# Performance work log

Hardware: AMD Instinct MI355X
Metric: run time of the kernel (lower is better)

The kernel has to match this reference:

```python
import jax, jax.numpy as jnp
import numpy as np

V, D, OUT, H, FF, L, K, POOL = 4097, 128, 64, 8, 256, 2, 9, 20
B, LE, LP = 32, 3000, 2000
GRID, WIDTH = 5, 257
DR = OUT // 8  # channel-attention reduction


def _ln(x, p):
    mu = jnp.mean(x, -1, keepdims=True)
    var = jnp.mean((x - mu) ** 2, -1, keepdims=True)
    return (x - mu) * jax.lax.rsqrt(var + 1e-5) * p[0] + p[1]


def _rope(x):
    # x: [B,H,S,hd], interleaved rotary embedding
    S, hd = x.shape[-2], x.shape[-1]
    inv = 1.0 / (10000.0 ** (jnp.arange(0, hd, 2, dtype=jnp.float32) / hd))
    ang = jnp.arange(S, dtype=jnp.float32)[:, None] * inv[None, :]  # [S,hd/2]
    c, s = jnp.cos(ang), jnp.sin(ang)
    x1, x2 = x[..., 0::2], x[..., 1::2]
    return jnp.stack([x1 * c - x2 * s, x1 * s + x2 * c], axis=-1).reshape(x.shape)


def _cbat_layer(x, qkv_w, qkv_b, o_w, o_b, ca_w1, ca_w2, sa_w,
                ff1_w, ff1_b, ff2_w, ff2_b, ln1, ln2):
    # x: [B,S,d] (batch-first inside CBAT, matching x.permute(1,0,2) in torch)
    Bx, S, d = x.shape
    hd = d // H

    def proj(i):
        return (x @ qkv_w[i] + qkv_b[i]).reshape(Bx, S, H, hd).transpose(0, 2, 1, 3)

    q, k, v = proj(0), proj(1), proj(2)
    q, k = _rope(q), _rope(k)
    attn = jax.nn.softmax(jnp.einsum('bhqd,bhkd->bhqk', q, k) / jnp.sqrt(jnp.float32(hd)), axis=-1)
    ctx = jnp.einsum('bhqk,bhkd->bhqd', attn, v).transpose(0, 2, 1, 3).reshape(Bx, S, d)
    # CBAM-style channel attention (pool over sequence)
    avg, mx = ctx.mean(1), ctx.max(1)  # [B,d]
    ca = jax.nn.sigmoid(jax.nn.relu(avg @ ca_w1) @ ca_w2 + jax.nn.relu(mx @ ca_w1) @ ca_w2)
    ctx = ctx * ca[:, None, :]
    # CBAM-style spatial attention (pool over channels, conv over sequence)
    feat = jnp.stack([ctx.mean(-1), ctx.max(-1)], axis=1)  # [B,2,S]
    sa = jax.nn.sigmoid(jax.lax.conv_general_dilated(
        feat, sa_w[None], (1,), 'SAME', dimension_numbers=('NCH', 'OIH', 'NCH')))  # [B,1,S]
    ctx = ctx * sa.transpose(0, 2, 1)
    out = ctx @ o_w + o_b
    aloss = jnp.mean(attn ** 2)  # adaptive attention regularizer
    x = _ln(x + out, ln1)
    ff = jax.nn.relu(x @ ff1_w + ff1_b) @ ff2_w + ff2_b
    x = _ln(x + ff, ln2)
    return x, aloss


def _mha(q_in, k_in, v_in, in_w, in_b, out_w, out_b):
    # torch nn.MultiheadAttention math (batch-first layout here; math identical)
    d = q_in.shape[-1]
    hd = d // H
    Wq, Wk, Wv = jnp.split(in_w, 3, 0)
    bq, bk, bv = jnp.split(in_b, 3, 0)

    def heads(t):
        return t.reshape(t.shape[0], t.shape[1], H, hd).transpose(0, 2, 1, 3)

    q, k, v = heads(q_in @ Wq.T + bq), heads(k_in @ Wk.T + bk), heads(v_in @ Wv.T + bv)
    attn = jax.nn.softmax(jnp.einsum('bhqd,bhkd->bhqk', q, k) / jnp.sqrt(jnp.float32(hd)), axis=-1)
    ctx = jnp.einsum('bhqk,bhkd->bhqd', attn, v).transpose(0, 2, 1, 3).reshape(q_in.shape)
    return ctx @ out_w.T + out_b


def _fourier(x, wc, ws, b):
    # FourierKAN layer: sum_k a*cos(kx) + b*sin(kx)
    kx = x[:, :, None] * jnp.arange(1, GRID + 1, dtype=x.dtype)  # [B,in,g]
    return jnp.einsum('big,oig->bo', jnp.cos(kx), wc) + jnp.einsum('big,oig->bo', jnp.sin(kx), ws) + b


def _frontend(ids, emb, conv_w, conv_b, bn):
    x = emb[ids]  # [B,Lseq,D]
    x = jax.lax.conv_general_dilated(x.transpose(0, 2, 1), conv_w, (1,), 'VALID',
                                     dimension_numbers=('NCH', 'OIH', 'NCH')) + conv_b[None, :, None]
    x = jax.nn.relu(x)
    x = jax.lax.reduce_window(x, -jnp.inf, jax.lax.max, (1, 1, POOL), (1, 1, POOL), 'VALID')
    g, be, mu, var = bn[0], bn[1], bn[2], bn[3]  # BatchNorm1d (eval mode)
    x = (x - mu[None, :, None]) * jax.lax.rsqrt(var[None, :, None] + 1e-5) * g[None, :, None] + be[None, :, None]
    return x.transpose(0, 2, 1)  # [B,S,OUT]


def _forward(enhancer_ids, promoter_ids, emb_en, emb_pr, conv_w_en, conv_b_en, conv_w_pr, conv_b_pr,
             bn_en, bn_pr, t_qkv_w, t_qkv_b, t_o_w, t_o_b, t_ca_w1, t_ca_w2, t_sa_w,
             t_ff1_w, t_ff1_b, t_ff2_w, t_ff2_b, t_ln1, t_ln2,
             cross_in_w, cross_in_b, cross_out_w, cross_out_b,
             self_in_w, self_in_b, self_out_w, self_out_b,
             fk1_c, fk1_s, fk1_b, fk2_c, fk2_s, fk2_b):
    en = _frontend(enhancer_ids, emb_en, conv_w_en, conv_b_en, bn_en)
    pr = _frontend(promoter_ids, emb_pr, conv_w_pr, conv_b_pr, bn_pr)
    total_aloss = jnp.float32(0.0)
    branches = [en, pr]
    for s in range(2):  # 0=enhancer stack, 1=promoter stack
        x = branches[s]
        for l in range(L):
            x, al = _cbat_layer(x, t_qkv_w[s, l], t_qkv_b[s, l], t_o_w[s, l], t_o_b[s, l],
                                t_ca_w1[s, l], t_ca_w2[s, l], t_sa_w[s, l],
                                t_ff1_w[s, l], t_ff1_b[s, l], t_ff2_w[s, l], t_ff2_b[s, l],
                                t_ln1[s, l], t_ln2[s, l])
            total_aloss = total_aloss + al
        branches[s] = x
    en, pr = branches
    en_att = _mha(en, pr, pr, cross_in_w, cross_in_b, cross_out_w, cross_out_b)
    en_fin = _mha(en_att, en_att, en_att, self_in_w, self_in_b, self_out_w, self_out_b)
    pr_fin = _mha(pr, pr, pr, self_in_w, self_in_b, self_out_w, self_out_b)
    combined = jnp.concatenate([en_fin.mean(1), pr_fin.mean(1)], axis=1)  # AdaptiveAvgPool1d(1)
    hidden = _fourier(combined, fk1_c, fk1_s, fk1_b)
    result = _fourier(hidden, fk2_c, fk2_s, fk2_b)
    return jax.nn.sigmoid(result), combined, total_aloss


def setup_inputs() -> dict:
    key = jax.random.key(0)
    ks = iter(jax.random.split(key, 64))

    def nrm(shape, sc=0.02):
        return jax.random.normal(next(ks), shape, jnp.float32) * sc

    ln_init = lambda: jnp.stack([jnp.ones((2, L, OUT)), jnp.zeros((2, L, OUT))], axis=2)
    inp = {
        'enhancer_ids': jax.random.randint(next(ks), (B, LE), 0, V),
        'promoter_ids': jax.random.randint(next(ks), (B, LP), 0, V),
        'enhancer_features': jax.random.normal(next(ks), (B, 10), jnp.float32),
        'promoter_features': jax.random.normal(next(ks), (B, 10), jnp.float32),
        'emb_en': nrm((V, D), 0.1), 'emb_pr': nrm((V, D), 0.1),
        'conv_w_en': nrm((OUT, D, K)), 'conv_b_en': jnp.zeros((OUT,)),
        'conv_w_pr': nrm((OUT, D, K)), 'conv_b_pr': jnp.zeros((OUT,)),
        'bn_en': jnp.stack([jnp.ones(OUT), jnp.zeros(OUT), jnp.zeros(OUT), jnp.ones(OUT)]),
        'bn_pr': jnp.stack([jnp.ones(OUT), jnp.zeros(OUT), jnp.zeros(OUT), jnp.ones(OUT)]),
        't_qkv_w': nrm((2, L, 3, OUT, OUT)), 't_qkv_b': jnp.zeros((2, L, 3, OUT)),
        't_o_w': nrm((2, L, OUT, OUT)), 't_o_b': jnp.zeros((2, L, OUT)),
        't_ca_w1': nrm((2, L, OUT, DR)), 't_ca_w2': nrm((2, L, DR, OUT)),
        't_sa_w': nrm((2, L, 2, 7)),
        't_ff1_w': nrm((2, L, OUT, FF)), 't_ff1_b': jnp.zeros((2, L, FF)),
        't_ff2_w': nrm((2, L, FF, OUT)), 't_ff2_b': jnp.zeros((2, L, OUT)),
        't_ln1': ln_init(), 't_ln2': ln_init(),
        'cross_in_w': nrm((3 * OUT, OUT)), 'cross_in_b': jnp.zeros((3 * OUT,)),
        'cross_out_w': nrm((OUT, OUT)), 'cross_out_b': jnp.zeros((OUT,)),
        'self_in_w': nrm((3 * OUT, OUT)), 'self_in_b': jnp.zeros((3 * OUT,)),
        'self_out_w': nrm((OUT, OUT)), 'self_out_b': jnp.zeros((OUT,)),
        'fk1_c': nrm((WIDTH, 2 * OUT, GRID), 0.1), 'fk1_s': nrm((WIDTH, 2 * OUT, GRID), 0.1),
        'fk1_b': jnp.zeros((WIDTH,)),
        'fk2_c': nrm((1, WIDTH, GRID), 0.1), 'fk2_s': nrm((1, WIDTH, GRID), 0.1),
        'fk2_b': jnp.zeros((1,)),
    }
    return inp


def reference(enhancer_ids, promoter_ids, enhancer_features, promoter_features,
              emb_en, emb_pr, conv_w_en, conv_b_en, conv_w_pr, conv_b_pr,
              bn_en, bn_pr, t_qkv_w, t_qkv_b, t_o_w, t_o_b, t_ca_w1, t_ca_w2, t_sa_w,
              t_ff1_w, t_ff1_b, t_ff2_w, t_ff2_b, t_ln1, t_ln2,
              cross_in_w, cross_in_b, cross_out_w, cross_out_b,
              self_in_w, self_in_b, self_out_w, self_out_b,
              fk1_c, fk1_s, fk1_b, fk2_c, fk2_s, fk2_b):
    # enhancer_features / promoter_features are accepted but unused by the original forward
    return _forward(enhancer_ids, promoter_ids, emb_en, emb_pr, conv_w_en, conv_b_en,
                    conv_w_pr, conv_b_pr, bn_en, bn_pr, t_qkv_w, t_qkv_b, t_o_w, t_o_b,
                    t_ca_w1, t_ca_w2, t_sa_w, t_ff1_w, t_ff1_b, t_ff2_w, t_ff2_b, t_ln1, t_ln2,
                    cross_in_w, cross_in_b, cross_out_w, cross_out_b,
                    self_in_w, self_in_b, self_out_w, self_out_b,
                    fk1_c, fk1_s, fk1_b, fk2_c, fk2_s, fk2_b)
```

## Files before the change

### kernel.cpp

```cpp
#include <hip/hip_runtime.h>
#include <math.h>

#define BB 32
#define SE 149
#define SP 99
#define LE_LEN 3000
#define LP_LEN 2000
#define VT 8
#define ROWS_EN (BB * SE)
#define ROWS_PR (BB * SP)
#define ROWS_ALL (ROWS_EN + ROWS_PR)

__device__ __forceinline__ void row_decode(int row, int& branch, int& b,
                                           int& s, int& S, int& lrow) {
  if (row < ROWS_EN) { branch = 0; S = SE; lrow = row; b = row / SE; s = row - b * SE; }
  else { branch = 1; S = SP; lrow = row - ROWS_EN; b = lrow / SP; s = lrow - b * SP; }
}

__global__ __launch_bounds__(256) void prep_kernel(
    const float* __restrict__ cw_en, const float* __restrict__ cw_pr,
    const float* __restrict__ cross_in, const float* __restrict__ cross_out,
    const float* __restrict__ self_in, const float* __restrict__ self_out,
    float* __restrict__ W2en, float* __restrict__ W2pr,
    float* __restrict__ Wt, float* __restrict__ Al) {
  int bb = blockIdx.x;
  if (bb == 0 && threadIdx.x == 0) Al[0] = 0.f;
  if (bb < 576) {
    const float* src = (bb < 288) ? cw_en : cw_pr;
    float* dst = (bb < 288) ? W2en : W2pr;
    int i = ((bb < 288) ? bb : bb - 288) * 256 + threadIdx.x;
    int oc = i / 1152, r = i % 1152, ic = r / 9, k = r % 9;
    dst[ic * 576 + k * 64 + oc] = src[i];
  } else {
    int m = bb - 576;
    const float* src = (m < 3) ? cross_in + m * 4096
                     : (m == 3) ? cross_out
                     : (m < 7) ? self_in + (m - 4) * 4096
                     : self_out;
    for (int i = threadIdx.x; i < 4096; i += 256) {
      int o = i >> 6, c = i & 63;
      Wt[m * 4096 + c * 64 + o] = src[i];
    }
  }
}
// ... 3 lines not shown
    const float* __restrict__ W2en, const float* __restrict__ W2pr,
    float* __restrict__ Cen, float* __restrict__ Cpr) {
  int blk = blockIdx.x;
  int branch = (blk >= 513);
  const float* emb = branch ? emb_pr : emb_en;
  const float* W2 = branch ? W2pr : W2en;
  float* C = branch ? Cpr : Cen;
  int v0 = (branch ? blk - 513 : blk) * VT;
  __shared__ float e[VT][128];
  int t = threadIdx.x;
  int nv = 4097 - v0; if (nv > VT) nv = VT;
  for (int i = t; i < nv * 128; i += 192) e[i >> 7][i & 127] = emb[v0 * 128 + i];
  __syncthreads();
  float a0[VT], a1[VT], a2[VT];
#pragma unroll
  for (int v = 0; v < VT; ++v) { a0[v] = 0.f; a1[v] = 0.f; a2[v] = 0.f; }
  for (int ic = 0; ic < 128; ++ic) {
    float w0 = W2[ic * 576 + t];
    float w1 = W2[ic * 576 + t + 192];
    float w2 = W2[ic * 576 + t + 384];
#pragma unroll
    for (int v = 0; v < VT; ++v) {
      float ev = e[v][ic];
      a0[v] += ev * w0; a1[v] += ev * w1; a2[v] += ev * w2;
    }
  }
  for (int v = 0; v < nv; ++v) {
    C[(size_t)(v0 + v) * 576 + t] = a0[v];
    C[(size_t)(v0 + v) * 576 + t + 192] = a1[v];
    C[(size_t)(v0 + v) * 576 + t + 384] = a2[v];
  }
}

__global__ __launch_bounds__(256) void frontend_kernel(
    const int* __restrict__ en_ids, const int* __restrict__ pr_ids,
    const float* __restrict__ Cen, const float* __restrict__ Cpr,
    const float* __restrict__ cb_en, const float* __restrict__ cb_pr,
    const float* __restrict__ bn_en, const float* __restrict__ bn_pr,
    float* __restrict__ Xen, float* __restrict__ Xpr) {
  int t = threadIdx.x;
  int wid = t >> 6, oc = t & 63;
  int row = blockIdx.x * 4 + wid;
  int branch, b, s, S, lrow;
  row_decode(row, branch, b, s, S, lrow);
  const int* ids = branch ? pr_ids : en_ids;
  int Lin = branch ? LP_LEN : LE_LEN;
  const float* C = branch ? Cpr : Cen;
  const float* cb = branch ? cb_pr : cb_en;
  const float* bn = branch ? bn_pr : bn_en;
  float* X = branch ? Xpr : Xen;
  __shared__ int idl[4][28];
  if (oc < 28) idl[wid][oc] = ids[b * Lin + s * 20 + oc];
  __syncthreads();
  float bias = cb[oc];
  float m = -INFINITY;
  for (int p = 0; p < 20; ++p) {
    float acc = bias;
#pragma unroll
    for (int k = 0; k < 9; ++k) acc += C[idl[wid][p + k] * 576 + k * 64 + oc];
    acc = fmaxf(acc, 0.f);
    m = fmaxf(m, acc);
  }
  float g = bn[oc], be = bn[64 + oc], mu = bn[128 + oc], var = bn[192 + oc];
  X[(size_t)lrow * 64 + oc] = (m - mu) * rsqrtf(var + 1e-5f) * g + be;
}

__global__ __launch_bounds__(256) void qkv_rope_kernel(
    const float* __restrict__ Xen, const float* __restrict__ Xpr,
    const float* __restrict__ t_qkv_w, const float* __restrict__ t_qkv_b, int l,
    float* __restrict__ Q, float* __restrict__ K, float* __restrict__ V) {
  int t = threadIdx.x;
  int wid = t >> 6, oc = t & 63;
  int row = blockIdx.x * 4 + wid;
  int branch, b, s, S, lrow;
  row_decode(row, branch, b, s, S, lrow);
  const float* X = branch ? Xpr : Xen;
  int idx = branch * 2 + l;
  const float* W = t_qkv_w + (size_t)idx * 3 * 4096;
  const float* bias = t_qkv_b + idx * 192;
  __shared__ float xr[4][64], qs[4][64], ks[4][64];
  xr[wid][oc] = X[lrow * 64 + oc];
  __syncthreads();
  float q = bias[oc], k = bias[64 + oc], v = bias[128 + oc];
  for (int c = 0; c < 64; ++c) {
    float xc = xr[wid][c];
    q += xc * W[c * 64 + oc];
    k += xc * W[4096 + c * 64 + oc];
    v += xc * W[8192 + c * 64 + oc];
  }
  qs[wid][oc] = q; ks[wid][oc] = k;
  V[row * 64 + oc] = v;
  __syncthreads();
  int j = oc & 7;
  int p = j >> 1;
  float inv = powf(10000.f, -(float)p * 0.25f);
  float ang = (float)s * inv;
  float cc = cosf(ang), ss = sinf(ang);
  float qo, ko;
  if ((j & 1) == 0) {
    qo = qs[wid][oc] * cc - qs[wid][oc + 1] * ss;
    ko = ks[wid][oc] * cc - ks[wid][oc + 1] * ss;
  } else {
    qo = qs[wid][oc - 1] * ss + qs[wid][oc] * cc;
    ko = ks[wid][oc - 1] * ss + ks[wid][oc] * cc;
  }
  Q[row * 64 + oc] = qo;
  K[row * 64 + oc] = ko;
}

__global__ __launch_bounds__(256) void attn_kernel(
    const float* __restrict__ Q, const float* __restrict__ K,
    const float* __restrict__ V, float* __restrict__ ctx,
    int nblk0, int Sq0, int Sk0, int qb0, int kb0, float als0,
    int Sq1, int Sk1, int qb1, int kb1, float als1,
    float* __restrict__ aloss_acc) {
  int blk = blockIdx.x;
// ... 24 lines not shown
      for (int j = 0; j < 8; ++j) sdot += q[j] * kk[kki * 8 + j];
      sdot *= sc;
      if (sdot > m) {
        float f = expf(m - sdot);
        sum *= f; sum2 *= f * f;
#pragma unroll
        for (int j = 0; j < 8; ++j) acc[j] *= f;
        m = sdot;
      }
      float e = expf(sdot - m);
      sum += e; sum2 += e * e;
#pragma unroll
      for (int j = 0; j < 8; ++j) acc[j] += e * vv[kki * 8 + j];
    }
    float invs = 1.f / sum;
#pragma unroll
    for (int j = 0; j < 8; ++j)
      ctx[(qb + b * Sq + t) * 64 + h * 8 + j] = acc[j] * invs;
    rowsum2 = sum2 * invs * invs;
  }
  if (als != 0.f) {
    float wsum = rowsum2;
    for (int off = 32; off; off >>= 1) wsum += __shfl_down(wsum, off, 64);
    __shared__ float wred[4];
    if ((t & 63) == 0) wred[t >> 6] = wsum;
    __syncthreads();
    if (t == 0) {
      float tot = wred[0] + wred[1] + wred[2] + wred[3];
      atomicAdd(aloss_acc, tot * als);
    }
  }
}

__global__ __launch_bounds__(512) void ca_kernel(
    const float* __restrict__ ctx, const float* __restrict__ t_ca_w1,
    const float* __restrict__ t_ca_w2, int l, float* __restrict__ ca) {
  int bp = blockIdx.x;
  int branch = bp >> 5, b = bp & 31;
  int S = branch ? SP : SE;
  int base = branch ? ROWS_EN : 0;
  int idx = branch * 2 + l;
  const float* W1 = t_ca_w1 + idx * 512;
  const float* W2 = t_ca_w2 + idx * 512;
  int t = threadIdx.x;
  int c = t & 63, seg = t >> 6;
  float sum = 0.f, mx = -INFINITY;
  for (int s = seg; s < S; s += 8) {
    float v = ctx[(base + b * S + s) * 64 + c];
    sum += v; mx = fmaxf(mx, v);
  }
  __shared__ float ssum[8][64], smx[8][64];
  ssum[seg][c] = sum; smx[seg][c] = mx;
  __syncthreads();
  __shared__ float avg_l[64], mx_l[64], ha[8], hm[8];
  if (t < 64) {
    float a = 0.f, m = -INFINITY;
#pragma unroll
    for (int g = 0; g < 8; ++g) { a += ssum[g][t]; m = fmaxf(m, smx[g][t]); }
    avg_l[t] = a / (float)S; mx_l[t] = m;
  }
  __syncthreads();
  if (t < 8) {
    float a = 0.f, m2 = 0.f;
    for (int i = 0; i < 64; ++i) {
      a += avg_l[i] * W1[i * 8 + t];
      m2 += mx_l[i] * W1[i * 8 + t];
    }
    ha[t] = fmaxf(a, 0.f); hm[t] = fmaxf(m2, 0.f);
  }
  __syncthreads();
  if (t < 64) {
    float o = 0.f;
#pragma unroll
    for (int j = 0; j < 8; ++j) o += (ha[j] + hm[j]) * W2[j * 64 + t];
    ca[bp * 64 + t] = 1.f / (1.f + expf(-o));
  }
}

__global__ __launch_bounds__(256) void feat_kernel(
    float* __restrict__ ctx, const float* __restrict__ ca,
    float* __restrict__ fmean, float* __restrict__ fmax) {
  int row = blockIdx.x * 4 + (threadIdx.x >> 6);
  int branch, b, s, S, lrow;
  row_decode(row, branch, b, s, S, lrow);
  int c = threadIdx.x & 63;
  float v = ctx[row * 64 + c] * ca[(branch * 32 + b) * 64 + c];
  ctx[row * 64 + c] = v;
  float sum = v, mx = v;
  for (int off = 32; off; off >>= 1) {
    sum += __shfl_xor(sum, off, 64);
    mx = fmaxf(mx, __shfl_xor(mx, off, 64));
  }
  if (c == 0) { fmean[row] = sum * (1.f / 64.f); fmax[row] = mx; }
}

__global__ __launch_bounds__(256) void tail_kernel(
    const float* __restrict__ ctx, const float* __restrict__ fmean,
    const float* __restrict__ fmax, const float* __restrict__ t_sa_w,
    const float* __restrict__ t_o_w, const float* __restrict__ t_o_b,
    const float* __restrict__ t_ln1, const float* __restrict__ t_ff1_w,
    const float* __restrict__ t_ff1_b, const float* __restrict__ t_ff2_w,
    const float* __restrict__ t_ff2_b, const float* __restrict__ t_ln2,
    int l, float* __restrict__ Xen, float* __restrict__ Xpr) {
  int t = threadIdx.x;
  int wid = t >> 6, lane = t & 63;
  int row = blockIdx.x * 4 + wid;
  int branch, b, s, S, lrow;
  row_decode(row, branch, b, s, S, lrow);
  int idx = branch * 2 + l;
  const float* sa_w = t_sa_w + idx * 14;
  float sa = 0.f;
  if (lane == 0) {
    for (int k = 0; k < 7; ++k) {
      int p = s + k - 3;
      if (p >= 0 && p < S)
        sa += fmean[row - s + p] * sa_w[k] + fmax[row - s + p] * sa_w[7 + k];
    }
    sa = 1.f / (1.f + expf(-sa));
  }
  sa = __shfl(sa, 0, 64);
  __shared__ float rowv[4][64], xr[4][64], h[4][256];
  rowv[wid][lane] = ctx[row * 64 + lane] * sa;
  __syncthreads();
  const float* o_w = t_o_w + (size_t)idx * 4096;
  float o = t_o_b[idx * 64 + lane];
  for (int c = 0; c < 64; ++c) o += rowv[wid][c] * o_w[c * 64 + lane];
  float* X = branch ? Xpr : Xen;
  float r = X[lrow * 64 + lane] + o;
  float mu = r;
  for (int of = 32; of; of >>= 1) mu += __shfl_xor(mu, of, 64);
  mu *= (1.f / 64.f);
  float d = r - mu;
  float var = d * d;
  for (int of = 32; of; of >>= 1) var += __shfl_xor(var, of, 64);
  var *= (1.f / 64.f);
  const float* ln1 = t_ln1 + idx * 128;
  float x1 = d * rsqrtf(var + 1e-5f) * ln1[lane] + ln1[64 + lane];
  xr[wid][lane] = x1;
  __syncthreads();
  const float* W1 = t_ff1_w + (size_t)idx * 16384;
  float a0 = t_ff1_b[idx * 256 + t], a1 = a0, a2 = a0, a3 = a0;
  for (int c = 0; c < 64; ++c) {
    float w = W1[c * 256 + t];
    a0 += xr[0][c] * w; a1 += xr[1][c] * w; a2 += xr[2][c] * w; a3 += xr[3][c] * w;
  }
  h[0][t] = fmaxf(a0, 0.f); h[1][t] = fmaxf(a1, 0.f);
  h[2][t] = fmaxf(a2, 0.f); h[3][t] = fmaxf(a3, 0.f);
  __syncthreads();
  const float* W2 = t_ff2_w + (size_t)idx * 16384;
  float o2 = t_ff2_b[idx * 64 + lane];
  for (int j = 0; j < 256; ++j) o2 += h[wid][j] * W2[j * 64 + lane];
  float r2 = x1 + o2;
  mu = r2;
  for (int of = 32; of; of >>= 1) mu += __shfl_xor(mu, of, 64);
  mu *= (1.f / 64.f);
  d = r2 - mu;
  var = d * d;
  for (int of = 32; of; of >>= 1) var += __shfl_xor(var, of, 64);
  var *= (1.f / 64.f);
  const float* ln2 = t_ln2 + idx * 128;
  X[lrow * 64 + lane] = d * rsqrtf(var + 1e-5f) * ln2[lane] + ln2[64 + lane];
}

__global__ __launch_bounds__(256) void cross_proj_kernel(
    const float* __restrict__ Xen, const float* __restrict__ Xpr,
    const float* __restrict__ Wt, const float* __restrict__ bias,
    float* __restrict__ Q, float* __restrict__ K, float* __restrict__ V) {
  int t = threadIdx.x;
  int wid = t >> 6, oc = t & 63;
  int blk = blockIdx.x;
  __shared__ float xr[4][64];
  if (blk < ROWS_EN / 4) {
    int row = blk * 4 + wid;
    xr[wid][oc] = Xen[row * 64 + oc];
    __syncthreads();
    float o = bias[oc];
    for (int c = 0; c < 64; ++c) o += xr[wid][c] * Wt[c * 64 + oc];
    Q[row * 64 + oc] = o;
  } else {
    int lr = (blk - ROWS_EN / 4) * 4 + wid;
    xr[wid][oc] = Xpr[lr * 64 + oc];
    __syncthreads();
    float k = bias[64 + oc], v = bias[128 + oc];
    for (int c = 0; c < 64; ++c) {
      float xc = xr[wid][c];
      k += xc * Wt[4096 + c * 64 + oc];
      v += xc * Wt[8192 + c * 64 + oc];
    }
    K[(ROWS_EN + lr) * 64 + oc] = k;
    V[(ROWS_EN + lr) * 64 + oc] = v;
  }
}

__global__ __launch_bounds__(256) void self_qkv_kernel(
    const float* __restrict__ inEn, const float* __restrict__ inPr,
    const float* __restrict__ Wt, const float* __restrict__ bias,
    float* __restrict__ Q, float* __restrict__ K, float* __restrict__ V) {
  int t = threadIdx.x;
  int wid = t >> 6, oc = t & 63;
  int row = blockIdx.x * 4 + wid;
  const float* in; int lrow;
  if (row < ROWS_EN) { in = inEn; lrow = row; }
  else { in = inPr; lrow = row - ROWS_EN; }
  __shared__ float xr[4][64];
  xr[wid][oc] = in[lrow * 64 + oc];
  __syncthreads();
  float q = bias[oc], k = bias[64 + oc], v = bias[128 + oc];
  for (int c = 0; c < 64; ++c) {
    float xc = xr[wid][c];
    q += xc * Wt[c * 64 + oc];
    k += xc * Wt[4096 + c * 64 + oc];
    v += xc * Wt[8192 + c * 64 + oc];
  }
  Q[row * 64 + oc] = q;
  K[row * 64 + oc] = k;
  V[row * 64 + oc] = v;
}

__global__ __launch_bounds__(256) void dual_proj_kernel(
    const float* __restrict__ in, const float* __restrict__ Wt,
    const float* __restrict__ bias, float* __restrict__ out0,
    float* __restrict__ out1) {
  int t = threadIdx.x;
  int wid = t >> 6, oc = t & 63;
  int row = blockIdx.x * 4 + wid;
  float* out; int lrow;
  if (row < ROWS_EN) { out = out0; lrow = row; }
  else { out = out1; lrow = row - ROWS_EN; }
  __shared__ float xr[4][64];
  xr[wid][oc] = in[row * 64 + oc];
  __syncthreads();
  float o = bias[oc];
  for (int c = 0; c < 64; ++c) o += xr[wid][c] * Wt[c * 64 + oc];
  out[lrow * 64 + oc] = o;
}

__global__ __launch_bounds__(512) void mean_trig_kernel(
    const float* __restrict__ en_fin, const float* __restrict__ pr_fin,
    float* __restrict__ comb, float* __restrict__ trig) {
  int b = blockIdx.x;
  int t = threadIdx.x;
  int col = t & 127, seg = t >> 7;
  float sum = 0.f;
  if (col < 64) {
    for (int s = seg; s < SE; s += 4) sum += en_fin[(b * SE + s) * 64 + col];
  } else {
    int c = col - 64;
    for (int s = seg; s < SP; s += 4) sum += pr_fin[(b * SP + s) * 64 + c];
  }
  __shared__ float red[4][128];
  __shared__ float comb_s[128];
  red[seg][col] = sum;
  __syncthreads();
  if (t < 128) {
    float tot = red[0][t] + red[1][t] + red[2][t] + red[3][t];
    float cv = tot / (t < 64 ? (float)SE : (float)SP);
    comb_s[t] = cv;
    comb[b * 128 + t] = cv;
  }
  __syncthreads();
  for (int i = t; i < 640; i += 512) {
    int ii = i / 5, g = i - ii * 5;
    float x = comb_s[ii] * (float)(g + 1);
    trig[b * 1280 + i] = cosf(x);
    trig[b * 1280 + 640 + i] = sinf(x);
  }
}

__global__ __launch_bounds__(256) void fourier1_kernel(
    const float* __restrict__ trig, const float* __restrict__ wc,
    const float* __restrict__ ws, const float* __restrict__ bias,
    float* __restrict__ hidden) {
  int b = blockIdx.x;
  int t = threadIdx.x;
  int wid = t >> 6, lane = t & 63;
  int o = blockIdx.y * 4 + wid;
  if (o >= 257) return;
  const float* ct = trig + b * 1280;
  const float* st = ct + 640;
  float acc = 0.f;
  for (int i = lane; i < 640; i += 64)
    acc += ct[i] * wc[o * 640 + i] + st[i] * ws[o * 640 + i];
  for (int off = 32; off; off >>= 1) acc += __shfl_xor(acc, off, 64);
  if (lane == 0) hidden[b * 257 + o] = acc + bias[o];
}

__global__ void fourier2_kernel(const float* __restrict__ hidden,
                                const float* __restrict__ wc,
                                const float* __restrict__ ws,
                                const float* __restrict__ bias,
                                const float* __restrict__ aloss_acc,
                                float* __restrict__ out) {
  int b = blockIdx.x;
  int t = threadIdx.x;
  float acc = 0.f;
  if (t < 257) {
    float x = hidden[b * 257 + t];
#pragma unroll
    for (int g = 0; g < 5; ++g) {
      float a = x * (float)(g + 1);
      acc += cosf(a) * wc[t * 5 + g] + sinf(a) * ws[t * 5 + g];
    }
  }
  for (int off = 32; off; off >>= 1) acc += __shfl_xor(acc, off, 64);
  __shared__ float wred[5];
  if ((t & 63) == 0) wred[t >> 6] = acc;
  __syncthreads();
  if (t == 0) {
    float tot = wred[0] + wred[1] + wred[2] + wred[3] + wred[4] + bias[0];
    out[b] = 1.f / (1.f + expf(-tot));
    if (b == 0) out[4128] = aloss_acc[0];
  }
}

extern "C" void kernel_launch(void* const* d_in, const int* in_sizes, int n_in,
                              void* d_out, int out_size, void* d_ws, size_t ws_size,
                              hipStream_t stream) {
  const int* en_ids = (const int*)d_in[0];
  const int* pr_ids = (const int*)d_in[1];
  const float* emb_en = (const float*)d_in[4];
  const float* emb_pr = (const float*)d_in[5];
  const float* conv_w_en = (const float*)d_in[6];
  const float* conv_b_en = (const float*)d_in[7];
  const float* conv_w_pr = (const float*)d_in[8];
  const float* conv_b_pr = (const float*)d_in[9];
  const float* bn_en = (const float*)d_in[10];
  const float* bn_pr = (const float*)d_in[11];
  const float* t_qkv_w = (const float*)d_in[12];
  const float* t_qkv_b = (const float*)d_in[13];
  const float* t_o_w = (const float*)d_in[14];
  const float* t_o_b = (const float*)d_in[15];
  const float* t_ca_w1 = (const float*)d_in[16];
  const float* t_ca_w2 = (const float*)d_in[17];
  const float* t_sa_w = (const float*)d_in[18];
  const float* t_ff1_w = (const float*)d_in[19];
  const float* t_ff1_b = (const float*)d_in[20];
  const float* t_ff2_w = (const float*)d_in[21];
  const float* t_ff2_b = (const float*)d_in[22];
  const float* t_ln1 = (const float*)d_in[23];
  const float* t_ln2 = (const float*)d_in[24];
  const float* cross_in_w = (const float*)d_in[25];
  const float* cross_in_b = (const float*)d_in[26];
  const float* cross_out_w = (const float*)d_in[27];
  const float* cross_out_b = (const float*)d_in[28];
  const float* self_in_w = (const float*)d_in[29];
  const float* self_in_b = (const float*)d_in[30];
  const float* self_out_w = (const float*)d_in[31];
  const float* self_out_b = (const float*)d_in[32];
  const float* fk1_c = (const float*)d_in[33];
  const float* fk1_s = (const float*)d_in[34];
  const float* fk1_b = (const float*)d_in[35];
  const float* fk2_c = (const float*)d_in[36];
  const float* fk2_s = (const float*)d_in[37];
  const float* fk2_b = (const float*)d_in[38];

  float* out = (float*)d_out;
  float* ws = (float*)d_ws;
  size_t off = 0;
  float* Cen = ws + off;  off += (size_t)4097 * 576;
  float* Cpr = ws + off;  off += (size_t)4097 * 576;
  float* W2en = ws + off; off += 73728;
  float* W2pr = ws + off; off += 73728;
  float* Wt = ws + off;   off += 8 * 4096;
  float* Xen = ws + off;  off += (size_t)ROWS_EN * 64;
  float* Xpr = ws + off;  off += (size_t)ROWS_PR * 64;
  float* Qb = ws + off;   off += (size_t)ROWS_ALL * 64;
  float* Kb = ws + off;   off += (size_t)ROWS_ALL * 64;
  float* Vb = ws + off;   off += (size_t)ROWS_ALL * 64;
  float* Ctx = ws + off;  off += (size_t)ROWS_ALL * 64;
  float* AttEn = ws + off; off += (size_t)ROWS_EN * 64;
  float* PrFin = ws + off; off += (size_t)ROWS_PR * 64;
  float* Fm = ws + off;   off += ROWS_ALL;
  float* Fx = ws + off;   off += ROWS_ALL;
  float* CaB = ws + off;  off += 2 * BB * 64;
  float* Hid = ws + off;  off += BB * 257;
  float* Trig = ws + off; off += (size_t)BB * 1280;
  float* Al = ws + off;   off += 8;

  const float als_en = 1.f / ((float)BB * 8.f * (float)SE * (float)SE);
  const float als_pr = 1.f / ((float)BB * 8.f * (float)SP * (float)SP);

  prep_kernel<<<584, 256, 0, stream>>>(conv_w_en, conv_w_pr, cross_in_w,
                                       cross_out_w, self_in_w, self_out_w,
                                       W2en, W2pr, Wt, Al);
  conv_table_kernel<<<1026, 192, 0, stream>>>(emb_en, emb_pr, W2en, W2pr, Cen, Cpr);
  frontend_kernel<<<ROWS_ALL / 4, 256, 0, stream>>>(en_ids, pr_ids, Cen, Cpr,
                                                    conv_b_en, conv_b_pr, bn_en,
                                                    bn_pr, Xen, Xpr);

  for (int l = 0; l < 2; ++l) {
    qkv_rope_kernel<<<ROWS_ALL / 4, 256, 0, stream>>>(Xen, Xpr, t_qkv_w,
                                                      t_qkv_b, l, Qb, Kb, Vb);
    attn_kernel<<<512, 256, 0, stream>>>(Qb, Kb, Vb, Ctx,
                                         256, SE, SE, 0, 0, als_en,
                                         SP, SP, ROWS_EN, ROWS_EN, als_pr, Al);
    ca_kernel<<<64, 512, 0, stream>>>(Ctx, t_ca_w1, t_ca_w2, l, CaB);
    feat_kernel<<<ROWS_ALL / 4, 256, 0, stream>>>(Ctx, CaB, Fm, Fx);
    tail_kernel<<<ROWS_ALL / 4, 256, 0, stream>>>(
        Ctx, Fm, Fx, t_sa_w, t_o_w, t_o_b, t_ln1, t_ff1_w, t_ff1_b,
        t_ff2_w, t_ff2_b, t_ln2, l, Xen, Xpr);
  }

  cross_proj_kernel<<<ROWS_ALL / 4, 256, 0, stream>>>(Xen, Xpr, Wt,
                                                      cross_in_b, Qb, Kb, Vb);
  attn_kernel<<<256, 256, 0, stream>>>(Qb, Kb, Vb, Ctx,
                                       256, SE, SP, 0, ROWS_EN, 0.f,
                                       0, 0, 0, 0, 0.f, Al);
  dual_proj_kernel<<<ROWS_EN / 4, 256, 0, stream>>>(Ctx, Wt + 3 * 4096,
                                                    cross_out_b, AttEn, AttEn);

  self_qkv_kernel<<<ROWS_ALL / 4, 256, 0, stream>>>(AttEn, Xpr, Wt + 4 * 4096,
                                                    self_in_b, Qb, Kb, Vb);
  attn_kernel<<<512, 256, 0, stream>>>(Qb, Kb, Vb, Ctx,
                                       256, SE, SE, 0, 0, 0.f,
                                       SP, SP, ROWS_EN, ROWS_EN, 0.f, Al);
  dual_proj_kernel<<<ROWS_ALL / 4, 256, 0, stream>>>(Ctx, Wt + 7 * 4096,
                                                     self_out_b, Xen, PrFin);

  mean_trig_kernel<<<BB, 512, 0, stream>>>(Xen, PrFin, out + 32, Trig);
  fourier1_kernel<<<dim3(BB, 65), 256, 0, stream>>>(Trig, fk1_c, fk1_s,
                                                    fk1_b, Hid);
  fourier2_kernel<<<BB, 320, 0, stream>>>(Hid, fk2_c, fk2_s, fk2_b, Al, out);
}
```

Baseline: 362.4 us.

## Fuse per-row projection kernels into neighbours and merge head kernels

Folds the QKV+RoPE projection into the frontend and tail kernels, and merges channel attention with the feature pass. It also computes promoter self-attention QKV early so the promoter self-attention runs in the same launch as the cross attention. The three classifier-head kernels are collapsed into one. The aim is fewer launches and fewer global round trips of intermediate activations. In exchange it adds larger workspace buffers, more register and shared-memory use per kernel, and per-batch serial work in the fused head and cafeat kernels.

Result: slower. 531.2 us (+46.6%).

```diff
diff --git a/kernel.cpp b/kernel.cpp
--- a/kernel.cpp
+++ b/kernel.cpp
@@ -10,6 +10,7 @@
 #define ROWS_EN (BB * SE)
 #define ROWS_PR (BB * SP)
 #define ROWS_ALL (ROWS_EN + ROWS_PR)
+#define ROWS_EXT (ROWS_ALL + ROWS_PR)
 
 __device__ __forceinline__ void row_decode(int row, int& branch, int& b,
                                            int& s, int& S, int& lrow) {
@@ -79,12 +80,14 @@
   }
 }
 
-__global__ __launch_bounds__(256) void frontend_kernel(
+__global__ __launch_bounds__(256) void frontqkv_kernel(
     const int* __restrict__ en_ids, const int* __restrict__ pr_ids,
     const float* __restrict__ Cen, const float* __restrict__ Cpr,
     const float* __restrict__ cb_en, const float* __restrict__ cb_pr,
     const float* __restrict__ bn_en, const float* __restrict__ bn_pr,
-    float* __restrict__ Xen, float* __restrict__ Xpr) {
+    const float* __restrict__ t_qkv_w, const float* __restrict__ t_qkv_b,
+    float* __restrict__ Xen, float* __restrict__ Xpr,
+    float* __restrict__ Q, float* __restrict__ K, float* __restrict__ V) {
   int t = threadIdx.x;
   int wid = t >> 6, oc = t & 63;
   int row = blockIdx.x * 4 + wid;
@@ -97,6 +100,7 @@
   const float* bn = branch ? bn_pr : bn_en;
   float* X = branch ? Xpr : Xen;
   __shared__ int idl[4][28];
+  __shared__ float xr[4][64], qs[4][64], ks[4][64];
   if (oc < 28) idl[wid][oc] = ids[b * Lin + s * 20 + oc];
   __syncthreads();
   float bias = cb[oc];
@@ -109,26 +113,14 @@
     m = fmaxf(m, acc);
   }
   float g = bn[oc], be = bn[64 + oc], mu = bn[128 + oc], var = bn[192 + oc];
-  X[(size_t)lrow * 64 + oc] = (m - mu) * rsqrtf(var + 1e-5f) * g + be;
-}
-
-__global__ __launch_bounds__(256) void qkv_rope_kernel(
-    const float* __restrict__ Xen, const float* __restrict__ Xpr,
-    const float* __restrict__ t_qkv_w, const float* __restrict__ t_qkv_b, int l,
-    float* __restrict__ Q, float* __restrict__ K, float* __restrict__ V) {
-  int t = threadIdx.x;
-  int wid = t >> 6, oc = t & 63;
-  int row = blockIdx.x * 4 + wid;
-  int branch, b, s, S, lrow;
-  row_decode(row, branch, b, s, S, lrow);
-  const float* X = branch ? Xpr : Xen;
-  int idx = branch * 2 + l;
+  float xv = (m - mu) * rsqrtf(var + 1e-5f) * g + be;
+  X[(size_t)lrow * 64 + oc] = xv;
+  xr[wid][oc] = xv;
+  __syncthreads();
+  int idx = branch * 2;
   const float* W = t_qkv_w + (size_t)idx * 3 * 4096;
-  const float* bias = t_qkv_b + idx * 192;
-  __shared__ float xr[4][64], qs[4][64], ks[4][64];
-  xr[wid][oc] = X[lrow * 64 + oc];
-  __syncthreads();
-  float q = bias[oc], k = bias[64 + oc], v = bias[128 + oc];
+  const float* qb_ = t_qkv_b + idx * 192;
+  float q = qb_[oc], k = qb_[64 + oc], v = qb_[128 + oc];
   for (int c = 0; c < 64; ++c) {
     float xc = xr[wid][c];
     q += xc * W[c * 64 + oc];
@@ -219,9 +211,10 @@
   }
 }
 
-__global__ __launch_bounds__(512) void ca_kernel(
-    const float* __restrict__ ctx, const float* __restrict__ t_ca_w1,
-    const float* __restrict__ t_ca_w2, int l, float* __restrict__ ca) {
+__global__ __launch_bounds__(512) void cafeat_kernel(
+    float* __restrict__ ctx, const float* __restrict__ t_ca_w1,
+    const float* __restrict__ t_ca_w2, int l,
+    float* __restrict__ fmean, float* __restrict__ fmax) {
   int bp = blockIdx.x;
   int branch = bp >> 5, b = bp & 31;
   int S = branch ? SP : SE;
@@ -233,13 +226,13 @@
   int c = t & 63, seg = t >> 6;
   float sum = 0.f, mx = -INFINITY;
   for (int s = seg; s < S; s += 8) {
-    float v = ctx[(base + b * S + s) * 64 + c];
+    float v = ctx[(size_t)(base + b * S + s) * 64 + c];
     sum += v; mx = fmaxf(mx, v);
   }
   __shared__ float ssum[8][64], smx[8][64];
   ssum[seg][c] = sum; smx[seg][c] = mx;
   __syncthreads();
-  __shared__ float avg_l[64], mx_l[64], ha[8], hm[8];
+  __shared__ float avg_l[64], mx_l[64], ha[8], hm[8], ca_s[64];
   if (t < 64) {
     float a = 0.f, m = -INFINITY;
 #pragma unroll
@@ -260,35 +253,33 @@
     float o = 0.f;
 #pragma unroll
     for (int j = 0; j < 8; ++j) o += (ha[j] + hm[j]) * W2[j * 64 + t];
-    ca[bp * 64 + t] = 1.f / (1.f + expf(-o));
-  }
-}
-
-__global__ __launch_bounds__(256) void feat_kernel(
-    float* __restrict__ ctx, const float* __restrict__ ca,
-    float* __restrict__ fmean, float* __restrict__ fmax) {
-  int row = blockIdx.x * 4 + (threadIdx.x >> 6);
-  int branch, b, s, S, lrow;
-  row_decode(row, branch, b, s, S, lrow);
-  int c = threadIdx.x & 63;
-  float v = ctx[row * 64 + c] * ca[(branch * 32 + b) * 64 + c];
-  ctx[row * 64 + c] = v;
-  float sum = v, mx = v;
-  for (int off = 32; off; off >>= 1) {
-    sum += __shfl_xor(sum, off, 64);
-    mx = fmaxf(mx, __shfl_xor(mx, off, 64));
-  }
-  if (c == 0) { fmean[row] = sum * (1.f / 64.f); fmax[row] = mx; }
-}
-
-__global__ __launch_bounds__(256) void tail_kernel(
+    ca_s[t] = 1.f / (1.f + expf(-o));
+  }
+  __syncthreads();
+  float cav = ca_s[c];
+  for (int s = seg; s < S; s += 8) {
+    int grow = base + b * S + s;
+    float v = ctx[(size_t)grow * 64 + c] * cav;
+    ctx[(size_t)grow * 64 + c] = v;
+    float su = v, mv = v;
+    for (int off = 32; off; off >>= 1) {
+      su += __shfl_xor(su, off, 64);
+      mv = fmaxf(mv, __shfl_xor(mv, off, 64));
+    }
+    if (c == 0) { fmean[grow] = su * (1.f / 64.f); fmax[grow] = mv; }
+  }
+}
+
+__global__ __launch_bounds__(256) void tailqkv_kernel(
     const float* __restrict__ ctx, const float* __restrict__ fmean,
     const float* __restrict__ fmax, const float* __restrict__ t_sa_w,
     const float* __restrict__ t_o_w, const float* __restrict__ t_o_b,
     const float* __restrict__ t_ln1, const float* __restrict__ t_ff1_w,
     const float* __restrict__ t_ff1_b, const float* __restrict__ t_ff2_w,
     const float* __restrict__ t_ff2_b, const float* __restrict__ t_ln2,
-    int l, float* __restrict__ Xen, float* __restrict__ Xpr) {
+    int l, float* __restrict__ Xen, float* __restrict__ Xpr,
+    const float* __restrict__ t_qkv_w, const float* __restrict__ t_qkv_b,
+    float* __restrict__ Q, float* __restrict__ K, float* __restrict__ V) {
   int t = threadIdx.x;
   int wid = t >> 6, lane = t & 63;
   int row = blockIdx.x * 4 + wid;
@@ -306,14 +297,14 @@
     sa = 1.f / (1.f + expf(-sa));
   }
   sa = __shfl(sa, 0, 64);
-  __shared__ float rowv[4][64], xr[4][64], h[4][256];
-  rowv[wid][lane] = ctx[row * 64 + lane] * sa;
+  __shared__ float rowv[4][64], xr[4][64], h[4][256], qs[4][64], ks[4][64];
+  rowv[wid][lane] = ctx[(size_t)row * 64 + lane] * sa;
   __syncthreads();
   const float* o_w = t_o_w + (size_t)idx * 4096;
   float o = t_o_b[idx * 64 + lane];
   for (int c = 0; c < 64; ++c) o += rowv[wid][c] * o_w[c * 64 + lane];
   float* X = branch ? Xpr : Xen;
-  float r = X[lrow * 64 + lane] + o;
+  float r = X[(size_t)lrow * 64 + lane] + o;
   float mu = r;
   for (int of = 32; of; of >>= 1) mu += __shfl_xor(mu, of, 64);
   mu *= (1.f / 64.f);
@@ -346,155 +337,241 @@
   for (int of = 32; of; of >>= 1) var += __shfl_xor(var, of, 64);
   var *= (1.f / 64.f);
   const float* ln2 = t_ln2 + idx * 128;
-  X[lrow * 64 + lane] = d * rsqrtf(var + 1e-5f) * ln2[lane] + ln2[64 + lane];
-}
-
-__global__ __launch_bounds__(256) void cross_proj_kernel(
-    const float* __restrict__ Xen, const float* __restrict__ Xpr,
-    const float* __restrict__ Wt, const float* __restrict__ bias,
+  float fv = d * rsqrtf(var + 1e-5f) * ln2[lane] + ln2[64 + lane];
+  X[(size_t)lrow * 64 + lane] = fv;
+  xr[wid][lane] = fv;
+  __syncthreads();
+  int idx2 = branch * 2 + l + 1;
+  const float* W = t_qkv_w + (size_t)idx2 * 3 * 4096;
+  const float* qb_ = t_qkv_b + idx2 * 192;
+  float q = qb_[lane], k = qb_[64 + lane], v = qb_[128 + lane];
+  for (int c = 0; c < 64; ++c) {
+    float xc = xr[wid][c];
+    q += xc * W[c * 64 + lane];
+    k += xc * W[4096 + c * 64 + lane];
+    v += xc * W[8192 + c * 64 + lane];
+  }
+  qs[wid][lane] = q; ks[wid][lane] = k;
+  V[(size_t)row * 64 + lane] = v;
+  __syncthreads();
+  int j = lane & 7;
+  int p = j >> 1;
+  float inv = powf(10000.f, -(float)p * 0.25f);
+  float ang = (float)s * inv;
+  float cc = cosf(ang), ss = sinf(ang);
+  float qo, ko;
+  if ((j & 1) == 0) {
+    qo = qs[wid][lane] * cc - qs[wid][lane + 1] * ss;
+    ko = ks[wid][lane] * cc - ks[wid][lane + 1] * ss;
+  } else {
+    qo = qs[wid][lane - 1] * ss + qs[wid][lane] * cc;
+    ko = ks[wid][lane - 1] * ss + ks[wid][lane] * cc;
+  }
+  Q[(size_t)row * 64 + lane] = qo;
+  K[(size_t)row * 64 + lane] = ko;
+}
+
+__global__ __launch_bounds__(256) void tailcross_kernel(
+    const float* __restrict__ ctx, const float* __restrict__ fmean,
+    const float* __restrict__ fmax, const float* __restrict__ t_sa_w,
+    const float* __restrict__ t_o_w, const float* __restrict__ t_o_b,
+    const float* __restrict__ t_ln1, const float* __restrict__ t_ff1_w,
+    const float* __restrict__ t_ff1_b, const float* __restrict__ t_ff2_w,
+    const float* __restrict__ t_ff2_b, const float* __restrict__ t_ln2,
+    float* __restrict__ Xen, float* __restrict__ Xpr,
+    const float* __restrict__ Wt, const float* __restrict__ cib,
+    const float* __restrict__ sib,
     float* __restrict__ Q, float* __restrict__ K, float* __restrict__ V) {
   int t = threadIdx.x;
-  int wid = t >> 6, oc = t & 63;
-  int blk = blockIdx.x;
-  __shared__ float xr[4][64];
-  if (blk < ROWS_EN / 4) {
-    int row = blk * 4 + wid;
-    xr[wid][oc] = Xen[row * 64 + oc];
-    __syncthreads();
-    float o = bias[oc];
-    for (int c = 0; c < 64; ++c) o += xr[wid][c] * Wt[c * 64 + oc];
-    Q[row * 64 + oc] = o;
+  int wid = t >> 6, lane = t & 63;
+  int row = blockIdx.x * 4 + wid;
+  int branch, b, s, S, lrow;
+  row_decode(row, branch, b, s, S, lrow);
+  int idx = branch * 2 + 1;
+  const float* sa_w = t_sa_w + idx * 14;
+  float sa = 0.f;
+  if (lane == 0) {
+    for (int k = 0; k < 7; ++k) {
+      int p = s + k - 3;
+      if (p >= 0 && p < S)
+        sa += fmean[row - s + p] * sa_w[k] + fmax[row - s + p] * sa_w[7 + k];
+    }
+    sa = 1.f / (1.f + expf(-sa));
+  }
+  sa = __shfl(sa, 0, 64);
+  __shared__ float rowv[4][64], xr[4][64], h[4][256];
+  rowv[wid][lane] = ctx[(size_t)row * 64 + lane] * sa;
+  __syncthreads();
+  const float* o_w = t_o_w + (size_t)idx * 4096;
+  float o = t_o_b[idx * 64 + lane];
+  for (int c = 0; c < 64; ++c) o += rowv[wid][c] * o_w[c * 64 + lane];
+  float* X = branch ? Xpr : Xen;
+  float r = X[(size_t)lrow * 64 + lane] + o;
+  float mu = r;
+  for (int of = 32; of; of >>= 1) mu += __shfl_xor(mu, of, 64);
+  mu *= (1.f / 64.f);
+  float d = r - mu;
+  float var = d * d;
+  for (int of = 32; of; of >>= 1) var += __shfl_xor(var, of, 64);
+  var *= (1.f / 64.f);
+  const float* ln1 = t_ln1 + idx * 128;
+  float x1 = d * rsqrtf(var + 1e-5f) * ln1[lane] + ln1[64 + lane];
+  xr[wid][lane] = x1;
+  __syncthreads();
+  const float* W1 = t_ff1_w + (size_t)idx * 16384;
+  float a0 = t_ff1_b[idx * 256 + t], a1 = a0, a2 = a0, a3 = a0;
+  for (int c = 0; c < 64; ++c) {
+    float w = W1[c * 256 + t];
+    a0 += xr[0][c] * w; a1 += xr[1][c] * w; a2 += xr[2][c] * w; a3 += xr[3][c] * w;
+  }
+  h[0][t] = fmaxf(a0, 0.f); h[1][t] = fmaxf(a1, 0.f);
+  h[2][t] = fmaxf(a2, 0.f); h[3][t] = fmaxf(a3, 0.f);
+  __syncthreads();
+  const float* W2 = t_ff2_w + (size_t)idx * 16384;
+  float o2 = t_ff2_b[idx * 64 + lane];
+  for (int j = 0; j < 256; ++j) o2 += h[wid][j] * W2[j * 64 + lane];
+  float r2 = x1 + o2;
+  mu = r2;
+  for (int of = 32; of; of >>= 1) mu += __shfl_xor(mu, of, 64);
+  mu *= (1.f / 64.f);
+  d = r2 - mu;
+  var = d * d;
+  for (int of = 32; of; of >>= 1) var += __shfl_xor(var, of, 64);
+  var *= (1.f / 64.f);
+  const float* ln2 = t_ln2 + idx * 128;
+  float fv = d * rsqrtf(var + 1e-5f) * ln2[lane] + ln2[64 + lane];
+  X[(size_t)lrow * 64 + lane] = fv;
+  xr[wid][lane] = fv;
+  __syncthreads();
+  if (branch == 0) {
+    float q = cib[lane];
+    for (int c = 0; c < 64; ++c) q += xr[wid][c] * Wt[c * 64 + lane];
+    Q[(size_t)row * 64 + lane] = q;
   } else {
-    int lr = (blk - ROWS_EN / 4) * 4 + wid;
-    xr[wid][oc] = Xpr[lr * 64 + oc];
-    __syncthreads();
-    float k = bias[64 + oc], v = bias[128 + oc];
+    float k = cib[64 + lane], v = cib[128 + lane];
+    float q2 = sib[lane], k2 = sib[64 + lane], v2 = sib[128 + lane];
     for (int c = 0; c < 64; ++c) {
       float xc = xr[wid][c];
-      k += xc * Wt[4096 + c * 64 + oc];
-      v += xc * Wt[8192 + c * 64 + oc];
-    }
-    K[(ROWS_EN + lr) * 64 + oc] = k;
-    V[(ROWS_EN + lr) * 64 + oc] = v;
-  }
-}
-
-__global__ __launch_bounds__(256) void self_qkv_kernel(
-    const float* __restrict__ inEn, const float* __restrict__ inPr,
-    const float* __restrict__ Wt, const float* __restrict__ bias,
+      k += xc * Wt[4096 + c * 64 + lane];
+      v += xc * Wt[8192 + c * 64 + lane];
+      q2 += xc * Wt[4 * 4096 + c * 64 + lane];
+      k2 += xc * Wt[5 * 4096 + c * 64 + lane];
+      v2 += xc * Wt[6 * 4096 + c * 64 + lane];
+    }
+    K[(size_t)(ROWS_EN + lrow) * 64 + lane] = k;
+    V[(size_t)(ROWS_EN + lrow) * 64 + lane] = v;
+    Q[(size_t)(ROWS_ALL + lrow) * 64 + lane] = q2;
+    K[(size_t)(ROWS_ALL + lrow) * 64 + lane] = k2;
+    V[(size_t)(ROWS_ALL + lrow) * 64 + lane] = v2;
+  }
+}
+
+__global__ __launch_bounds__(256) void crossout_selfqkv_kernel(
+    const float* __restrict__ ctx, const float* __restrict__ Wt,
+    const float* __restrict__ cob, const float* __restrict__ sib,
     float* __restrict__ Q, float* __restrict__ K, float* __restrict__ V) {
   int t = threadIdx.x;
-  int wid = t >> 6, oc = t & 63;
+  int wid = t >> 6, lane = t & 63;
   int row = blockIdx.x * 4 + wid;
-  const float* in; int lrow;
-  if (row < ROWS_EN) { in = inEn; lrow = row; }
-  else { in = inPr; lrow = row - ROWS_EN; }
+  __shared__ float xr[4][64], att[4][64];
+  xr[wid][lane] = ctx[(size_t)row * 64 + lane];
+  __syncthreads();
+  float o = cob[lane];
+  for (int c = 0; c < 64; ++c) o += xr[wid][c] * Wt[3 * 4096 + c * 64 + lane];
+  att[wid][lane] = o;
+  __syncthreads();
+  float q = sib[lane], k = sib[64 + lane], v = sib[128 + lane];
+  for (int c = 0; c < 64; ++c) {
+    float xc = att[wid][c];
+    q += xc * Wt[4 * 4096 + c * 64 + lane];
+    k += xc * Wt[5 * 4096 + c * 64 + lane];
+    v += xc * Wt[6 * 4096 + c * 64 + lane];
+  }
+  Q[(size_t)row * 64 + lane] = q;
+  K[(size_t)row * 64 + lane] = k;
+  V[(size_t)row * 64 + lane] = v;
+}
+
+__global__ __launch_bounds__(256) void final_out_kernel(
+    const float* __restrict__ ctx, const float* __restrict__ Wt,
+    const float* __restrict__ sob, float* __restrict__ Xen,
+    float* __restrict__ PrFin) {
+  int t = threadIdx.x;
+  int wid = t >> 6, lane = t & 63;
+  int row = blockIdx.x * 4 + wid;
+  const float* src;
+  float* dst;
+  int lrow;
+  if (row < ROWS_EN) { src = ctx + (size_t)row * 64; dst = Xen; lrow = row; }
+  else { lrow = row - ROWS_EN; src = ctx + (size_t)(ROWS_ALL + lrow) * 64; dst = PrFin; }
   __shared__ float xr[4][64];
-  xr[wid][oc] = in[lrow * 64 + oc];
-  __syncthreads();
-  float q = bias[oc], k = bias[64 + oc], v = bias[128 + oc];
-  for (int c = 0; c < 64; ++c) {
-    float xc = xr[wid][c];
-    q += xc * Wt[c * 64 + oc];
-    k += xc * Wt[4096 + c * 64 + oc];
-    v += xc * Wt[8192 + c * 64 + oc];
-  }
-  Q[row * 64 + oc] = q;
-  K[row * 64 + oc] = k;
-  V[row * 64 + oc] = v;
-}
-
-__global__ __launch_bounds__(256) void dual_proj_kernel(
-    const float* __restrict__ in, const float* __restrict__ Wt,
-    const float* __restrict__ bias, float* __restrict__ out0,
-    float* __restrict__ out1) {
-  int t = threadIdx.x;
-  int wid = t >> 6, oc = t & 63;
-  int row = blockIdx.x * 4 + wid;
-  float* out; int lrow;
-  if (row < ROWS_EN) { out = out0; lrow = row; }
-  else { out = out1; lrow = row - ROWS_EN; }
-  __shared__ float xr[4][64];
-  xr[wid][oc] = in[row * 64 + oc];
-  __syncthreads();
-  float o = bias[oc];
-  for (int c = 0; c < 64; ++c) o += xr[wid][c] * Wt[c * 64 + oc];
-  out[lrow * 64 + oc] = o;
-}
-
-__global__ __launch_bounds__(512) void mean_trig_kernel(
+  xr[wid][lane] = src[lane];
+  __syncthreads();
+  float o = sob[lane];
+  for (int c = 0; c < 64; ++c) o += xr[wid][c] * Wt[7 * 4096 + c * 64 + lane];
+  dst[(size_t)lrow * 64 + lane] = o;
+}
+
+__global__ __launch_bounds__(512) void headfuse_kernel(
     const float* __restrict__ en_fin, const float* __restrict__ pr_fin,
-    float* __restrict__ comb, float* __restrict__ trig) {
+    const float* __restrict__ wc1, const float* __restrict__ ws1,
+    const float* __restrict__ b1, const float* __restrict__ wc2,
+    const float* __restrict__ ws2, const float* __restrict__ b2,
+    const float* __restrict__ aloss_acc, float* __restrict__ out) {
   int b = blockIdx.x;
   int t = threadIdx.x;
-  int col = t & 127, seg = t >> 7;
-  float sum = 0.f;
-  if (col < 64) {
-    for (int s = seg; s < SE; s += 4) sum += en_fin[(b * SE + s) * 64 + col];
-  } else {
-    int c = col - 64;
-    for (int s = seg; s < SP; s += 4) sum += pr_fin[(b * SP + s) * 64 + c];
-  }
-  __shared__ float red[4][128];
-  __shared__ float comb_s[128];
-  red[seg][col] = sum;
+  __shared__ float red[4][128], comb_s[128], ct[640], st[640], hid[257], wred[8];
+  {
+    int col = t & 127, seg = t >> 7;
+    float sum = 0.f;
+    if (col < 64) {
+      for (int s = seg; s < SE; s += 4) sum += en_fin[(size_t)(b * SE + s) * 64 + col];
+    } else {
+      int c = col - 64;
+      for (int s = seg; s < SP; s += 4) sum += pr_fin[(size_t)(b * SP + s) * 64 + c];
+    }
+    red[seg][col] = sum;
+  }
   __syncthreads();
   if (t < 128) {
     float tot = red[0][t] + red[1][t] + red[2][t] + red[3][t];
     float cv = tot / (t < 64 ? (float)SE : (float)SP);
     comb_s[t] = cv;
-    comb[b * 128 + t] = cv;
+    out[32 + b * 128 + t] = cv;
   }
   __syncthreads();
   for (int i = t; i < 640; i += 512) {
     int ii = i / 5, g = i - ii * 5;
     float x = comb_s[ii] * (float)(g + 1);
-    trig[b * 1280 + i] = cosf(x);
-    trig[b * 1280 + 640 + i] = sinf(x);
-  }
-}
-
-__global__ __launch_bounds__(256) void fourier1_kernel(
-    const float* __restrict__ trig, const float* __restrict__ wc,
-    const float* __restrict__ ws, const float* __restrict__ bias,
-    float* __restrict__ hidden) {
-  int b = blockIdx.x;
-  int t = threadIdx.x;
-  int wid = t >> 6, lane = t & 63;
-  int o = blockIdx.y * 4 + wid;
-  if (o >= 257) return;
-  const float* ct = trig + b * 1280;
-  const float* st = ct + 640;
-  float acc = 0.f;
-  for (int i = lane; i < 640; i += 64)
-    acc += ct[i] * wc[o * 640 + i] + st[i] * ws[o * 640 + i];
-  for (int off = 32; off; off >>= 1) acc += __shfl_xor(acc, off, 64);
-  if (lane == 0) hidden[b * 257 + o] = acc + bias[o];
-}
-
-__global__ void fourier2_kernel(const float* __restrict__ hidden,
-                                const float* __restrict__ wc,
-                                const float* __restrict__ ws,
-                                const float* __restrict__ bias,
-                                const float* __restrict__ aloss_acc,
-                                float* __restrict__ out) {
-  int b = blockIdx.x;
-  int t = threadIdx.x;
+    ct[i] = cosf(x);
+    st[i] = sinf(x);
+  }
+  __syncthreads();
+  int w = t >> 6, lane = t & 63;
+  for (int o = w; o < 257; o += 8) {
+    float acc = 0.f;
+    for (int i = lane; i < 640; i += 64)
+      acc += ct[i] * wc1[(size_t)o * 640 + i] + st[i] * ws1[(size_t)o * 640 + i];
+    for (int off = 32; off; off >>= 1) acc += __shfl_xor(acc, off, 64);
+    if (lane == 0) hid[o] = acc + b1[o];
+  }
+  __syncthreads();
   float acc = 0.f;
   if (t < 257) {
-    float x = hidden[b * 257 + t];
+    float x = hid[t];
 #pragma unroll
     for (int g = 0; g < 5; ++g) {
       float a = x * (float)(g + 1);
-      acc += cosf(a) * wc[t * 5 + g] + sinf(a) * ws[t * 5 + g];
+      acc += cosf(a) * wc2[t * 5 + g] + sinf(a) * ws2[t * 5 + g];
     }
   }
   for (int off = 32; off; off >>= 1) acc += __shfl_xor(acc, off, 64);
-  __shared__ float wred[5];
-  if ((t & 63) == 0) wred[t >> 6] = acc;
+  if (lane == 0) wred[w] = acc;
   __syncthreads();
   if (t == 0) {
-    float tot = wred[0] + wred[1] + wred[2] + wred[3] + wred[4] + bias[0];
+    float tot = b2[0];
+#pragma unroll
+    for (int g = 0; g < 8; ++g) tot += wred[g];
     out[b] = 1.f / (1.f + expf(-tot));
     if (b == 0) out[4128] = aloss_acc[0];
   }
@@ -551,17 +628,13 @@
   float* Wt = ws + off;   off += 8 * 4096;
   float* Xen = ws + off;  off += (size_t)ROWS_EN * 64;
   float* Xpr = ws + off;  off += (size_t)ROWS_PR * 64;
-  float* Qb = ws + off;   off += (size_t)ROWS_ALL * 64;
-  float* Kb = ws + off;   off += (size_t)ROWS_ALL * 64;
-  float* Vb = ws + off;   off += (size_t)ROWS_ALL * 64;
-  float* Ctx = ws + off;  off += (size_t)ROWS_ALL * 64;
-  float* AttEn = ws + off; off += (size_t)ROWS_EN * 64;
+  float* Qb = ws + off;   off += (size_t)ROWS_EXT * 64;
+  float* Kb = ws + off;   off += (size_t)ROWS_EXT * 64;
+  float* Vb = ws + off;   off += (size_t)ROWS_EXT * 64;
+  float* Ctx = ws + off;  off += (size_t)ROWS_EXT * 64;
   float* PrFin = ws + off; off += (size_t)ROWS_PR * 64;
   float* Fm = ws + off;   off += ROWS_ALL;
   float* Fx = ws + off;   off += ROWS_ALL;
-  float* CaB = ws + off;  off += 2 * BB * 64;
-  float* Hid = ws + off;  off += BB * 257;
-  float* Trig = ws + off; off += (size_t)BB * 1280;
   float* Al = ws + off;   off += 8;
 
   const float als_en = 1.f / ((float)BB * 8.f * (float)SE * (float)SE);
@@ -571,41 +644,37 @@
                                        cross_out_w, self_in_w, self_out_w,
                                        W2en, W2pr, Wt, Al);
   conv_table_kernel<<<1026, 192, 0, stream>>>(emb_en, emb_pr, W2en, W2pr, Cen, Cpr);
-  frontend_kernel<<<ROWS_ALL / 4, 256, 0, stream>>>(en_ids, pr_ids, Cen, Cpr,
-                                                    conv_b_en, conv_b_pr, bn_en,
-                                                    bn_pr, Xen, Xpr);
+  frontqkv_kernel<<<ROWS_ALL / 4, 256, 0, stream>>>(
+      en_ids, pr_ids, Cen, Cpr, conv_b_en, conv_b_pr, bn_en, bn_pr,
+      t_qkv_w, t_qkv_b, Xen, Xpr, Qb, Kb, Vb);
 
   for (int l = 0; l < 2; ++l) {
-    qkv_rope_kernel<<<ROWS_ALL / 4, 256, 0, stream>>>(Xen, Xpr, t_qkv_w,
-                                                      t_qkv_b, l, Qb, Kb, Vb);
     attn_kernel<<<512, 256, 0, stream>>>(Qb, Kb, Vb, Ctx,
                                          256, SE, SE, 0, 0, als_en,
                                          SP, SP, ROWS_EN, ROWS_EN, als_pr, Al);
-    ca_kernel<<<64, 512, 0, stream>>>(Ctx, t_ca_w1, t_ca_w2, l, CaB);
-    feat_kernel<<<ROWS_ALL / 4, 256, 0, stream>>>(Ctx, CaB, Fm, Fx);
-    tail_kernel<<<ROWS_ALL / 4, 256, 0, stream>>>(
-        Ctx, Fm, Fx, t_sa_w, t_o_w, t_o_b, t_ln1, t_ff1_w, t_ff1_b,
-        t_ff2_w, t_ff2_b, t_ln2, l, Xen, Xpr);
-  }
-
-  cross_proj_kernel<<<ROWS_ALL / 4, 256, 0, stream>>>(Xen, Xpr, Wt,
-                                                      cross_in_b, Qb, Kb, Vb);
+    cafeat_kernel<<<64, 512, 0, stream>>>(Ctx, t_ca_w1, t_ca_w2, l, Fm, Fx);
+    if (l == 0) {
+      tailqkv_kernel<<<ROWS_ALL / 4, 256, 0, stream>>>(
+          Ctx, Fm, Fx, t_sa_w, t_o_w, t_o_b, t_ln1, t_ff1_w, t_ff1_b,
+          t_ff2_w, t_ff2_b, t_ln2, l, Xen, Xpr, t_qkv_w, t_qkv_b, Qb, Kb, Vb);
+    } else {
+      tailcross_kernel<<<ROWS_ALL / 4, 256, 0, stream>>>(
+          Ctx, Fm, Fx, t_sa_w, t_o_w, t_o_b, t_ln1, t_ff1_w, t_ff1_b,
+          t_ff2_w, t_ff2_b, t_ln2, Xen, Xpr, Wt, cross_in_b, self_in_b,
+          Qb, Kb, Vb);
+    }
+  }
+
+  attn_kernel<<<512, 256, 0, stream>>>(Qb, Kb, Vb, Ctx,
+                                       256, SE, SP, 0, ROWS_EN, 0.f,
+                                       SP, SP, ROWS_ALL, ROWS_ALL, 0.f, Al);
+  crossout_selfqkv_kernel<<<ROWS_EN / 4, 256, 0, stream>>>(
+      Ctx, Wt, cross_out_b, self_in_b, Qb, Kb, Vb);
   attn_kernel<<<256, 256, 0, stream>>>(Qb, Kb, Vb, Ctx,
-                                       256, SE, SP, 0, ROWS_EN, 0.f,
+                                       256, SE, SE, 0, 0, 0.f,
                                        0, 0, 0, 0, 0.f, Al);
-  dual_proj_kernel<<<ROWS_EN / 4, 256, 0, stream>>>(Ctx, Wt + 3 * 4096,
-                                                    cross_out_b, AttEn, AttEn);
-
-  self_qkv_kernel<<<ROWS_ALL / 4, 256, 0, stream>>>(AttEn, Xpr, Wt + 4 * 4096,
-                                                    self_in_b, Qb, Kb, Vb);
-  attn_kernel<<<512, 256, 0, stream>>>(Qb, Kb, Vb, Ctx,
-                                       256, SE, SE, 0, 0, 0.f,
-                                       SP, SP, ROWS_EN, ROWS_EN, 0.f, Al);
-  dual_proj_kernel<<<ROWS_ALL / 4, 256, 0, stream>>>(Ctx, Wt + 7 * 4096,
-                                                     self_out_b, Xen, PrFin);
-
-  mean_trig_kernel<<<BB, 512, 0, stream>>>(Xen, PrFin, out + 32, Trig);
-  fourier1_kernel<<<dim3(BB, 65), 256, 0, stream>>>(Trig, fk1_c, fk1_s,
-                                                    fk1_b, Hid);
-  fourier2_kernel<<<BB, 320, 0, stream>>>(Hid, fk2_c, fk2_s, fk2_b, Al, out);
-}
+  final_out_kernel<<<ROWS_ALL / 4, 256, 0, stream>>>(Ctx, Wt, self_out_b,
+                                                     Xen, PrFin);
+  headfuse_kernel<<<BB, 512, 0, stream>>>(Xen, PrFin, fk1_c, fk1_s, fk1_b,
+                                          fk2_c, fk2_s, fk2_b, Al, out);
+}
```
